# Performance work log

Hardware: AMD Instinct MI355X
Metric: run time of the kernel (lower is better)

The kernel has to match this reference:

```python
import jax, jax.numpy as jnp
import numpy as np

DIM = 1536
NH = 12
HD = DIM // NH          # 128
C = HD // 2             # 64 rotary pairs
F, H, W = 6, 20, 20
L = F * H * W           # 2400
B = 1
MAX_POS = 1024
EPS = 1e-6


def _rope_freqs():
    """[MAX_POS, C, 2, 2] rotation matrices, split [22,21,21] across f/h/w axes."""
    c0 = C - 2 * (C // 3)           # 22
    c1 = C // 3                      # 21
    pos = np.arange(MAX_POS, dtype=np.float32)
    parts = []
    for m in (c0, c1, c1):
        inv = 1.0 / (10000.0 ** (np.arange(m, dtype=np.float32) / m))
        parts.append(pos[:, None] * inv[None, :])
    ang = np.concatenate(parts, axis=1)          # [MAX_POS, C]
    cos, sin = np.cos(ang), np.sin(ang)
    # R[..., j, k]: rows [cos, -sin], [sin, cos]
    R = np.stack([np.stack([cos, -sin], -1), np.stack([sin, cos], -1)], -2)
    return jnp.asarray(R, dtype=jnp.float32)


def setup_inputs() -> dict:
    key = jax.random.key(0)
    ks = jax.random.split(key, 12)
    s = 1.0 / np.sqrt(DIM)
    lin = lambda k: (jax.random.normal(k, (DIM, DIM), jnp.float32) * s)
    return {
        "x": jax.random.normal(ks[0], (B, L, DIM), jnp.float32),
        "Wq": lin(ks[1]), "bq": jax.random.normal(ks[2], (DIM,), jnp.float32) * 0.01,
        "Wk": lin(ks[3]), "bk": jax.random.normal(ks[4], (DIM,), jnp.float32) * 0.01,
        "Wv": lin(ks[5]), "bv": jax.random.normal(ks[6], (DIM,), jnp.float32) * 0.01,
        "Wo": lin(ks[7]), "bo": jax.random.normal(ks[8], (DIM,), jnp.float32) * 0.01,
        "gq": jnp.ones((DIM,), jnp.float32),
        "gk": jnp.ones((DIM,), jnp.float32),
        "seq_lens": jnp.full((B,), L, dtype=jnp.int32),
        "grid_sizes": jnp.asarray([[F, H, W]], dtype=jnp.int32),
        "freqs": _rope_freqs(),
    }


def _rms_norm(x, g, eps=EPS):
    # WanRMSNorm: x * rsqrt(mean(x^2, -1) + eps) * weight
    return x * jax.lax.rsqrt(jnp.mean(jnp.square(x), axis=-1, keepdims=True) + eps) * g


def _rope_apply(xh, grid_sizes, freqs):
    """xh: [B, L, n, d]; freqs: [MAX_POS, c, 2, 2]. All samples share one grid."""
    b, l, n, d = xh.shape
    c = d // 2
    c0 = c - 2 * (c // 3)
    c1 = c // 3
    f, h, w = (int(v) for v in np.asarray(grid_sizes[0]))
    # build per-position 3D rotation matrices: [f*h*w, c, 2, 2]
    fa = jnp.broadcast_to(freqs[:f, :c0][:, None, None], (f, h, w, c0, 2, 2))
    fb = jnp.broadcast_to(freqs[:h, c0:c0 + c1][None, :, None], (f, h, w, c1, 2, 2))
    fc = jnp.broadcast_to(freqs[:w, c0 + c1:c][None, None, :], (f, h, w, c1, 2, 2))
    R = jnp.concatenate([fa, fb, fc], axis=3).reshape(f * h * w, c, 2, 2)
    xp = xh.reshape(b, l, n, c, 2)
    out = jnp.einsum('lcjk,blnck->blncj', R, xp)
    return out.reshape(b, l, n, d)


def reference(x, Wq, bq, Wk, bk, Wv, bv, Wo, bo, gq, gk, seq_lens, grid_sizes, freqs):
    b, l = x.shape[:2]
    q = _rms_norm(x @ Wq.T + bq, gq).reshape(b, l, NH, HD)
    k = _rms_norm(x @ Wk.T + bk, gk).reshape(b, l, NH, HD)
    v = (x @ Wv.T + bv).reshape(b, l, NH, HD)
    q = _rope_apply(q, grid_sizes, freqs)
    k = _rope_apply(k, grid_sizes, freqs)
    # full attention with key-length mask (window_size=(-1,-1))
    scores = jnp.einsum('bqnd,bknd->bnqk', q, k) / np.sqrt(HD)
    kmask = jnp.arange(l)[None, :] < seq_lens[:, None]          # [B, L]
    scores = jnp.where(kmask[:, None, None, :], scores, -1e9)
    attn = jax.nn.softmax(scores, axis=-1)
    out = jnp.einsum('bnqk,bknd->bqnd', attn, v).reshape(b, l, DIM)
    return out @ Wo.T + bo
```

## Files before the change

### kernel.cpp

```cpp
#include <hip/hip_runtime.h>
#include <hip/hip_bf16.h>
#include <stdint.h>


#define DIM  1536
#define NH   12
#define HD   128
#define LSEQ 2400
#define LPAD 2432
#define KT2  32
#define NT2  (LPAD / KT2)
#define NTH  38
#define KVH  (LPAD / 2)

typedef __attribute__((ext_vector_type(8))) short short8;
typedef __attribute__((ext_vector_type(8))) _Float16 half8;
typedef __attribute__((ext_vector_type(4))) float f32x4;
typedef unsigned short ushort_t;
typedef unsigned int   uint32;

__device__ __forceinline__ ushort_t f2bf(float f) {
  union { float f; unsigned u; } v; v.f = f;
  unsigned r = (v.u + 0x7fffu + ((v.u >> 16) & 1u)) >> 16;
  return (ushort_t)r;
}
__device__ __forceinline__ float bf2f(ushort_t h) {
  union { unsigned u; float f; } v; v.u = ((unsigned)h) << 16;
  return v.f;
}
__device__ __forceinline__ void async16(void* lds, const void* g) {
  __builtin_amdgcn_global_load_lds(
      (const __attribute__((address_space(1))) uint32*)g,
      (__attribute__((address_space(3))) uint32*)lds, 16, 0, 0);
}
__device__ __forceinline__ uint4 pack8(const float* f) {
  uint4 u;
  u.x = (uint32)f2bf(f[0]) | ((uint32)f2bf(f[1]) << 16);
  u.y = (uint32)f2bf(f[2]) | ((uint32)f2bf(f[3]) << 16);
  u.z = (uint32)f2bf(f[4]) | ((uint32)f2bf(f[5]) << 16);
  u.w = (uint32)f2bf(f[6]) | ((uint32)f2bf(f[7]) << 16);
  return u;
}

__global__ void cvt_all(const float* __restrict__ x,
                        const float* __restrict__ W0, const float* __restrict__ W1,
                        const float* __restrict__ W2, const float* __restrict__ W3,
                        ushort_t* __restrict__ xd,
                        ushort_t* __restrict__ d0, ushort_t* __restrict__ d1,
                        ushort_t* __restrict__ d2, ushort_t* __restrict__ d3)
{
  const int z = blockIdx.y;
  const int i = blockIdx.x * 256 + threadIdx.x;
  if (z == 0) {
    uint4 u = {0, 0, 0, 0};
    if (i * 8 < LSEQ * DIM) {
      float f[8];
      *(float4*)f = *(const float4*)(x + i * 8);
      *(float4*)(f + 4) = *(const float4*)(x + i * 8 + 4);
      u = pack8(f);
    }
    *(uint4*)(xd + i * 8) = u;
    return;
  }
  if (blockIdx.x >= DIM * DIM / 2048) return;
  const float* s = (z == 1) ? W0 : ((z == 2) ? W1 : ((z == 3) ? W2 : W3));
  ushort_t* d    = (z == 1) ? d0 : ((z == 2) ? d1 : ((z == 3) ? d2 : d3));
  float f[8];
  *(float4*)f = *(const float4*)(s + i * 8);
  *(float4*)(f + 4) = *(const float4*)(s + i * 8 + 4);
  *(uint4*)(d + i * 8) = pack8(f);
}

template<int OUT_F32>
__global__ __launch_bounds__(256) void gemm_bt(
    const ushort_t* __restrict__ Ap,
    const ushort_t* __restrict__ B0, const ushort_t* __restrict__ B1, const ushort_t* __restrict__ B2,
    const float* __restrict__ b0, const float* __restrict__ b1, const float* __restrict__ b2,
    void* __restrict__ D0, void* __restrict__ D1, void* __restrict__ D2,
    int Mout)
{
  const int z = blockIdx.y;
  const ushort_t* Bw  = (z == 0) ? B0 : ((z == 1) ? B1 : B2);
  const float* bias   = (z == 0) ? b0 : ((z == 1) ? b1 : b2);
  void* D             = (z == 0) ? D0 : ((z == 1) ? D1 : D2);

  const int bm = blockIdx.x / 12, bn = blockIdx.x % 12;
  const int tid = threadIdx.x;
  const int w = tid >> 6, lam = tid & 63;
  const int wr = w >> 1, wc = w & 1;
  const int lane15 = lam & 15, quad = lam >> 4;

  __shared__ __align__(16) char lds[32768];
  char* sA = lds;
  char* sB = lds + 16384;

  f32x4 acc[4][4];
#pragma unroll
  for (int i = 0; i < 4; ++i)
#pragma unroll
    for (int j = 0; j < 4; ++j) acc[i][j] = {};

  const int sm = (w * 32) + (lam >> 3);
  const int sc = (lam & 7);

  for (int k0 = 0; k0 < DIM; k0 += 64) {
    __syncthreads();
#pragma unroll
    for (int i = 0; i < 4; ++i) {
      const int li = w * 4096 + i * 1024;
      const int m = sm + i * 8;
      const int c = sc ^ (m & 7);
      async16(sA + li, Ap + (size_t)(bm * 128 + m) * DIM + k0 + c * 8);
      async16(sB + li, Bw + (size_t)(bn * 128 + m) * DIM + k0 + c * 8);
    }
    __syncthreads();
#pragma unroll
    for (int kc = 0; kc < 2; ++kc) {
      const int chunk = kc * 4 + quad;
      short8 af[4], bfr[4];
#pragma unroll
      for (int i = 0; i < 4; ++i) {
        const int m = wr * 64 + i * 16 + lane15;
        af[i] = *(const short8*)(sA + m * 128 + ((chunk ^ (m & 7)) * 16));
      }
#pragma unroll
      for (int j = 0; j < 4; ++j) {
        const int n = wc * 64 + j * 16 + lane15;
        bfr[j] = *(const short8*)(sB + n * 128 + ((chunk ^ (n & 7)) * 16));
      }
#pragma unroll
      for (int i = 0; i < 4; ++i)
#pragma unroll
        for (int j = 0; j < 4; ++j)
          acc[i][j] = __builtin_amdgcn_mfma_f32_16x16x32_bf16(af[i], bfr[j], acc[i][j], 0, 0, 0);
    }
  }

#pragma unroll
  for (int j = 0; j < 4; ++j) {
    const int n = bn * 128 + wc * 64 + j * 16 + lane15;
    const float bv = bias[n];
#pragma unroll
    for (int i = 0; i < 4; ++i) {
      const int mb = bm * 128 + wr * 64 + i * 16 + quad * 4;
#pragma unroll
      for (int r = 0; r < 4; ++r) {
        const int m = mb + r;
        const float val = acc[i][j][r] + bv;
        if (OUT_F32) {
          if (m < Mout) ((float*)D)[(size_t)m * DIM + n] = val;
        } else {
          ((ushort_t*)D)[(size_t)m * DIM + n] = f2bf(val);
        }
      }
    }
  }
}

__global__ __launch_bounds__(256) void nr_vp(
    const ushort_t* __restrict__ qpre, const ushort_t* __restrict__ kpre,
    const ushort_t* __restrict__ vbf,
    const float* __restrict__ gq, const float* __restrict__ gk,
    const float* __restrict__ freqs,
    const int* __restrict__ seq_lens, const int* __restrict__ grid_sizes,
    ushort_t* __restrict__ qh, ushort_t* __restrict__ kh,
    ushort_t* __restrict__ vp)
{
  const int bx = blockIdx.x;
  const int tid = threadIdx.x;
  __shared__ float wsum[4];
  __shared__ float srstd;
  __shared__ ushort_t tbuf[32][33];

  if (bx >= 2 * LPAD) {
    const int vb = bx - 2 * LPAD;
    const int head = vb / (NT2 * 4);
    const int rem = vb - head * (NT2 * 4);
    const int t2 = rem >> 2;
    const int d0 = (rem & 3) * 32;
    const int l0 = t2 * 32;
    const int tx = tid & 31, ty = tid >> 5;
#pragma unroll
    for (int rr = 0; rr < 4; ++rr)
      tbuf[ty * 4 + rr][tx] = vbf[(size_t)(l0 + ty * 4 + rr) * DIM + head * HD + d0 + tx];
    __syncthreads();
#pragma unroll
    for (int rr = 0; rr < 4; ++rr) {
      const int d = d0 + ty * 4 + rr;
      vp[(((size_t)head * NT2 + t2) * HD + d) * KT2 + tx] = tbuf[tx][ty * 4 + rr];
    }
    return;
  }

  const int row = bx >> 1;
  const int which = bx & 1;
  const ushort_t* src = which ? kpre : qpre;
  const float* g = which ? gk : gq;
  ushort_t* dst = which ? kh : qh;

  float s = 0.f;
  if (tid < 192) {
    uint4 u = *(const uint4*)(src + (size_t)row * DIM + tid * 8);
    const uint32 uu[4] = {u.x, u.y, u.z, u.w};
#pragma unroll
    for (int i = 0; i < 4; ++i) {
      float a = bf2f((ushort_t)(uu[i] & 0xffff));
      float b = bf2f((ushort_t)(uu[i] >> 16));
      s += a * a + b * b;
    }
  }
#pragma unroll
  for (int off = 32; off; off >>= 1) s += __shfl_down(s, off, 64);
  if ((tid & 63) == 0) wsum[tid >> 6] = s;
  __syncthreads();
  if (tid == 0)
    srstd = rsqrtf((wsum[0] + wsum[1] + wsum[2] + wsum[3]) / (float)DIM + 1e-6f);
  __syncthreads();
  const float rstd = srstd;

  const int seq = seq_lens[0];
  const int h_ = grid_sizes[1], w_ = grid_sizes[2];
  const int hw = h_ * w_;
  const int fidx = row / hw;
  const int rem = row - fidx * hw;
  const int hidx = rem / w_;
  const int widx = rem - hidx * w_;
  const bool live = row < seq;

#pragma unroll
  for (int pp = 0; pp < 3; ++pp) {
    const int p = tid + pp * 256;
    const int c = p & 63, head = p >> 6;
    const int e_in = head * HD + 2 * c;
    uint32 xin = *(const uint32*)(src + (size_t)row * DIM + e_in);
    float x0 = bf2f((ushort_t)(xin & 0xffff));
    float x1 = bf2f((ushort_t)(xin >> 16));
    float2 gg = *(const float2*)(g + e_in);
    float y0 = x0 * rstd * gg.x, y1 = x1 * rstd * gg.y;
    const int pos = (c < 22) ? fidx : ((c < 43) ? hidx : widx);
    float4 R = *(const float4*)(freqs + ((size_t)pos * 64 + c) * 4);
    float o0 = R.x * y0 + R.y * y1;
    float o1 = R.z * y0 + R.w * y1;
    uint32 op = live ? ((uint32)f2bf(o0) | ((uint32)f2bf(o1) << 16)) : 0u;
    *(uint32*)(dst + ((size_t)head * LPAD + row) * HD + 2 * c) = op;
  }
}

__global__ __launch_bounds__(256, 2) void attn6(
    const ushort_t* __restrict__ qh, const ushort_t* __restrict__ kh,
    const ushort_t* __restrict__ vp, const int* __restrict__ seq_lens,
    _Float16* __restrict__ opA, _Float16* __restrict__ opB,
    float* __restrict__ lp)
{
  const int half = blockIdx.z;
  const int head = blockIdx.y;
  const int q0 = blockIdx.x * 64;
  const int tid = threadIdx.x;
  const int w = tid >> 6, lam = tid & 63;
  const int lane15 = lam & 15, quad = lam >> 4;
  const int seq = seq_lens[0];
  _Float16* op = half ? opB : opA;

  __shared__ __align__(16) char kbuf[2][8192];
  __shared__ __align__(16) char vbuf[2][8192];
  __shared__ __align__(16) ushort_t pbuf[4][16][40];

  const ushort_t* qbase = qh + ((size_t)head * LPAD + q0 + w * 16) * HD;
  short8 qf[4];
#pragma unroll
  for (int kc = 0; kc < 4; ++kc)
    qf[kc] = *(const short8*)(qbase + lane15 * HD + kc * 32 + quad * 8);

  f32x4 o[8];
#pragma unroll
  for (int dt = 0; dt < 8; ++dt) o[dt] = {};
  float lacc[4] = {0.f, 0.f, 0.f, 0.f};

  const float scale = 0.08838834764831845f;

  const ushort_t* khh = kh + (size_t)head * LPAD * HD;
  const ushort_t* vph = vp + (size_t)head * NT2 * HD * KT2;

  const int krow0 = w * 8 + (lam >> 4);
  const int kslot = lam & 15;
  const int vrow0 = w * 32 + (lam >> 2);
  const int vslot = lam & 3;

#define STAGE(gt, b)                                                     \
  {                                                                      \
    const ushort_t* kg = khh + (size_t)(gt) * (KT2 * HD);                \
    const ushort_t* vg = vph + (size_t)(gt) * (HD * KT2);                \
    _Pragma("unroll")                                                    \
    for (int i = 0; i < 2; ++i) {                                        \
      const int li = w * 2048 + i * 1024;                                \
      const int kr = krow0 + i * 4;                                      \
      const int kc_ = kslot ^ (kr & 15);                                 \
      async16(kbuf[b] + li, kg + kr * HD + kc_ * 8);                     \
      const int vr = vrow0 + i * 16;                                     \
      const int vc = vslot ^ (vr & 3);                                   \
      async16(vbuf[b] + li, vg + vr * KT2 + vc * 8);                     \
    }                                                                    \
  }

  STAGE(half * NTH, 0)
  __syncthreads();

  for (int t = 0; t < NTH; ++t) {
    const int b = t & 1;
    const int gt = half * NTH + t;
    if (t + 1 < NTH) STAGE(gt + 1, b ^ 1)

    f32x4 S[2];
    S[0] = {}; S[1] = {};
#pragma unroll
    for (int n0 = 0; n0 < 2; ++n0)
#pragma unroll
      for (int kc = 0; kc < 4; ++kc) {
        short8 kf = *(const short8*)(kbuf[b] + (n0 * 16 + lane15) * 256 +
                                     (((kc * 4 + quad) ^ lane15) * 16));
        S[n0] = __builtin_amdgcn_mfma_f32_16x16x32_bf16(qf[kc], kf, S[n0], 0, 0, 0);
      }

#pragma unroll
    for (int n0 = 0; n0 < 2; ++n0) {
      const bool valid = (gt * KT2 + n0 * 16 + lane15) < seq;
#pragma unroll
      for (int r = 0; r < 4; ++r) {
        float e = valid ? __expf(S[n0][r] * scale - 12.0f) : 0.f;
        lacc[r] += e;
        pbuf[w][quad * 4 + r][n0 * 16 + lane15] = f2bf(e);
      }
    }
    asm volatile("s_waitcnt lgkmcnt(0)" ::: "memory");

    short8 pf = *(const short8*)(&pbuf[w][lane15][quad * 8]);
#pragma unroll
    for (int dt = 0; dt < 8; ++dt) {
      short8 vf = *(const short8*)(vbuf[b] + (dt * 16 + lane15) * 64 +
                                   ((quad ^ (lane15 & 3)) * 16));
      o[dt] = __builtin_amdgcn_mfma_f32_16x16x32_bf16(pf, vf, o[dt], 0, 0, 0);
    }
    __syncthreads();
  }
#undef STAGE

  float lrow[4], linv[4];
#pragma unroll
  for (int r = 0; r < 4; ++r) {
    float l = lacc[r];
#pragma unroll
    for (int off = 1; off < 16; off <<= 1) l += __shfl_xor(l, off, 16);
    lrow[r] = l;
    linv[r] = 1.0f / l;
  }
  if (lane15 == 0) {
#pragma unroll
    for (int r = 0; r < 4; ++r)
      lp[((size_t)half * NH + head) * LPAD + q0 + w * 16 + quad * 4 + r] = lrow[r];
  }
#pragma unroll
  for (int dt = 0; dt < 8; ++dt)
#pragma unroll
    for (int r = 0; r < 4; ++r) {
      const int m = q0 + w * 16 + quad * 4 + r;
      op[(size_t)m * DIM + head * HD + dt * 16 + lane15] =
          (_Float16)(o[dt][r] * linv[r]);
    }
}

__global__ void merge(const _Float16* __restrict__ oA, const _Float16* __restrict__ oB,
                      const float* __restrict__ lp, ushort_t* __restrict__ attno)
{
  const int i = blockIdx.x * 256 + threadIdx.x;
  const int e = i * 8;
  const int m = e / DIM;
  const int head = (e - m * DIM) >> 7;
  const float lA = lp[(size_t)head * LPAD + m];
  const float lB = lp[((size_t)NH + head) * LPAD + m];
  const float inv = 1.0f / (lA + lB);
  const float wA = lA * inv, wB = lB * inv;
  half8 a = *(const half8*)(oA + e);
  half8 b = *(const half8*)(oB + e);
  float f[8];
#pragma unroll
  for (int j = 0; j < 8; ++j) f[j] = (float)a[j] * wA + (float)b[j] * wB;
  *(uint4*)(attno + e) = pack8(f);
}

extern "C" void kernel_launch(void* const* d_in, const int* in_sizes, int n_in,
                              void* d_out, int out_size, void* d_ws, size_t ws_size,
                              hipStream_t stream)
{
  const float* x  = (const float*)d_in[0];
  const float* Wq = (const float*)d_in[1];
  const float* bq = (const float*)d_in[2];
  const float* Wk = (const float*)d_in[3];
  const float* bk = (const float*)d_in[4];
  const float* Wv = (const float*)d_in[5];
  const float* bv = (const float*)d_in[6];
  const float* Wo = (const float*)d_in[7];
  const float* bo = (const float*)d_in[8];
  const float* gq = (const float*)d_in[9];
  const float* gk = (const float*)d_in[10];
  const int* seq_lens   = (const int*)d_in[11];
  const int* grid_sizes = (const int*)d_in[12];
  const float* freqs    = (const float*)d_in[13];
  float* out = (float*)d_out;

  const size_t BUF = (size_t)LPAD * DIM * 2;
  const size_t WB  = (size_t)DIM * DIM * 2;
  char* ws = (char*)d_ws;
  dim3 blk(256);

  ushort_t* xbf  = (ushort_t*)(ws);
  ushort_t* wqb  = (ushort_t*)(ws + BUF);
  ushort_t* wkb  = (ushort_t*)(ws + BUF + WB);
  ushort_t* wvb  = (ushort_t*)(ws + BUF + 2 * WB);
  ushort_t* wob  = (ushort_t*)(ws + BUF + 3 * WB);
  ushort_t* qpre = (ushort_t*)(ws + BUF + 4 * WB);
  ushort_t* kpre = (ushort_t*)(ws + 2 * BUF + 4 * WB);
  ushort_t* qh   = (ushort_t*)(ws + 3 * BUF + 4 * WB);
  ushort_t* kh   = (ushort_t*)(ws + 4 * BUF + 4 * WB);
  ushort_t* vbf  = (ushort_t*)(ws + 5 * BUF + 4 * WB);
  ushort_t* vp    = xbf;
  ushort_t* attno = xbf;
  _Float16* opA = (_Float16*)qpre;
  _Float16* opB = (_Float16*)vbf;
  float*    lp  = (float*)wvb;

  cvt_all<<<dim3(LPAD * DIM / 2048, 5), blk, 0, stream>>>(
      x, Wq, Wk, Wv, Wo, xbf, wqb, wkb, wvb, wob);
  gemm_bt<0><<<dim3(228, 3), blk, 0, stream>>>(
      xbf, wqb, wkb, wvb, bq, bk, bv, qpre, kpre, vbf, 0);
  nr_vp<<<dim3(2 * LPAD + NH * NT2 * 4), blk, 0, stream>>>(
      qpre, kpre, vbf, gq, gk, freqs, seq_lens, grid_sizes, qh, kh, vp);
  attn6<<<dim3(LPAD / 64, NH, 2), blk, 0, stream>>>(
      qh, kh, vp, seq_lens, opA, opB, lp);
  merge<<<dim3(LPAD * DIM / 2048), blk, 0, stream>>>(opA, opB, lp, attno);
  gemm_bt<1><<<dim3(228, 1), blk, 0, stream>>>(
      attno, wob, wob, wob, bo, bo, bo, out, out, out, LSEQ);
}
```

Before: 296.9 us.

## Double query tile per wave and split keys into four chunks

```diff
diff --git a/kernel.cpp b/kernel.cpp
--- a/kernel.cpp
+++ b/kernel.cpp
@@ -10,8 +10,7 @@
 #define LPAD 2432
 #define KT2  32
 #define NT2  (LPAD / KT2)
-#define NTH  38
-#define KVH  (LPAD / 2)
+#define NTQ  19
 
 typedef __attribute__((ext_vector_type(8))) short short8;
 typedef __attribute__((ext_vector_type(8))) _Float16 half8;
@@ -246,35 +245,40 @@
   }
 }
 
-__global__ __launch_bounds__(256, 2) void attn6(
+__global__ __launch_bounds__(256, 3) void attn7(
     const ushort_t* __restrict__ qh, const ushort_t* __restrict__ kh,
     const ushort_t* __restrict__ vp, const int* __restrict__ seq_lens,
-    _Float16* __restrict__ opA, _Float16* __restrict__ opB,
+    _Float16* __restrict__ op0, _Float16* __restrict__ op1,
+    _Float16* __restrict__ op2, _Float16* __restrict__ op3,
     float* __restrict__ lp)
 {
-  const int half = blockIdx.z;
+  const int qz = blockIdx.z;
   const int head = blockIdx.y;
-  const int q0 = blockIdx.x * 64;
+  const int q0 = blockIdx.x * 128;
   const int tid = threadIdx.x;
   const int w = tid >> 6, lam = tid & 63;
   const int lane15 = lam & 15, quad = lam >> 4;
   const int seq = seq_lens[0];
-  _Float16* op = half ? opB : opA;
+  _Float16* op = (qz == 0) ? op0 : ((qz == 1) ? op1 : ((qz == 2) ? op2 : op3));
 
   __shared__ __align__(16) char kbuf[2][8192];
   __shared__ __align__(16) char vbuf[2][8192];
-  __shared__ __align__(16) ushort_t pbuf[4][16][40];
-
-  const ushort_t* qbase = qh + ((size_t)head * LPAD + q0 + w * 16) * HD;
-  short8 qf[4];
-#pragma unroll
-  for (int kc = 0; kc < 4; ++kc)
-    qf[kc] = *(const short8*)(qbase + lane15 * HD + kc * 32 + quad * 8);
-
-  f32x4 o[8];
-#pragma unroll
-  for (int dt = 0; dt < 8; ++dt) o[dt] = {};
-  float lacc[4] = {0.f, 0.f, 0.f, 0.f};
+  __shared__ __align__(16) ushort_t pbuf[4][32][40];
+
+  const ushort_t* qbase = qh + ((size_t)head * LPAD + q0 + w * 32) * HD;
+  short8 qf[2][4];
+#pragma unroll
+  for (int qt = 0; qt < 2; ++qt)
+#pragma unroll
+    for (int kc = 0; kc < 4; ++kc)
+      qf[qt][kc] = *(const short8*)(qbase + (qt * 16 + lane15) * HD + kc * 32 + quad * 8);
+
+  f32x4 o[2][8];
+#pragma unroll
+  for (int qt = 0; qt < 2; ++qt)
+#pragma unroll
+    for (int dt = 0; dt < 8; ++dt) o[qt][dt] = {};
+  float lacc[2][4] = {};
 
   const float scale = 0.08838834764831845f;
 
@@ -283,8 +287,6 @@
 
   const int krow0 = w * 8 + (lam >> 4);
   const int kslot = lam & 15;
-  const int vrow0 = w * 32 + (lam >> 2);
-  const int vslot = lam & 3;
 
 #define STAGE(gt, b)                                                     \
   {                                                                      \
@@ -296,94 +298,114 @@
       const int kr = krow0 + i * 4;                                      \
       const int kc_ = kslot ^ (kr & 15);                                 \
       async16(kbuf[b] + li, kg + kr * HD + kc_ * 8);                     \
-      const int vr = vrow0 + i * 16;                                     \
-      const int vc = vslot ^ (vr & 3);                                   \
-      async16(vbuf[b] + li, vg + vr * KT2 + vc * 8);                     \
+      const int G = w * 128 + i * 64 + lam;                              \
+      const int l_ = (G >> 2) & 15;                                      \
+      const int cc = (G & 3) ^ (l_ & 3);                                 \
+      const int d_ = ((G >> 6) << 4) + l_;                               \
+      async16(vbuf[b] + li, vg + d_ * KT2 + cc * 8);                     \
     }                                                                    \
   }
 
-  STAGE(half * NTH, 0)
+  const int tbase = qz * NTQ;
+  STAGE(tbase, 0)
   __syncthreads();
 
-  for (int t = 0; t < NTH; ++t) {
+  for (int t = 0; t < NTQ; ++t) {
     const int b = t & 1;
-    const int gt = half * NTH + t;
-    if (t + 1 < NTH) STAGE(gt + 1, b ^ 1)
-
-    f32x4 S[2];
-    S[0] = {}; S[1] = {};
+    const int gt = tbase + t;
+    if (t + 1 < NTQ) STAGE(gt + 1, b ^ 1)
+
+    f32x4 S[2][2];
+    S[0][0] = {}; S[0][1] = {}; S[1][0] = {}; S[1][1] = {};
 #pragma unroll
     for (int n0 = 0; n0 < 2; ++n0)
 #pragma unroll
       for (int kc = 0; kc < 4; ++kc) {
         short8 kf = *(const short8*)(kbuf[b] + (n0 * 16 + lane15) * 256 +
                                      (((kc * 4 + quad) ^ lane15) * 16));
-        S[n0] = __builtin_amdgcn_mfma_f32_16x16x32_bf16(qf[kc], kf, S[n0], 0, 0, 0);
+#pragma unroll
+        for (int qt = 0; qt < 2; ++qt)
+          S[qt][n0] = __builtin_amdgcn_mfma_f32_16x16x32_bf16(qf[qt][kc], kf, S[qt][n0], 0, 0, 0);
       }
 
 #pragma unroll
     for (int n0 = 0; n0 < 2; ++n0) {
       const bool valid = (gt * KT2 + n0 * 16 + lane15) < seq;
 #pragma unroll
+      for (int qt = 0; qt < 2; ++qt)
+#pragma unroll
+        for (int r = 0; r < 4; ++r) {
+          float e = valid ? __expf(S[qt][n0][r] * scale - 12.0f) : 0.f;
+          lacc[qt][r] += e;
+          pbuf[w][qt * 16 + quad * 4 + r][n0 * 16 + lane15] = f2bf(e);
+        }
+    }
+    asm volatile("s_waitcnt lgkmcnt(0)" ::: "memory");
+
+    short8 pf[2];
+#pragma unroll
+    for (int qt = 0; qt < 2; ++qt)
+      pf[qt] = *(const short8*)(&pbuf[w][qt * 16 + lane15][quad * 8]);
+#pragma unroll
+    for (int dt = 0; dt < 8; ++dt) {
+      short8 vf = *(const short8*)(vbuf[b] + dt * 1024 +
+                                   (lane15 * 4 + (quad ^ (lane15 & 3))) * 16);
+#pragma unroll
+      for (int qt = 0; qt < 2; ++qt)
+        o[qt][dt] = __builtin_amdgcn_mfma_f32_16x16x32_bf16(pf[qt], vf, o[qt][dt], 0, 0, 0);
+    }
+    __syncthreads();
+  }
+#undef STAGE
+
+#pragma unroll
+  for (int qt = 0; qt < 2; ++qt) {
+    float lrow[4], linv[4];
+#pragma unroll
+    for (int r = 0; r < 4; ++r) {
+      float l = lacc[qt][r];
+#pragma unroll
+      for (int off = 1; off < 16; off <<= 1) l += __shfl_xor(l, off, 16);
+      lrow[r] = l;
+      linv[r] = 1.0f / l;
+    }
+    if (lane15 == 0) {
+#pragma unroll
+      for (int r = 0; r < 4; ++r)
+        lp[((size_t)qz * NH + head) * LPAD + q0 + w * 32 + qt * 16 + quad * 4 + r] = lrow[r];
+    }
+#pragma unroll
+    for (int dt = 0; dt < 8; ++dt)
+#pragma unroll
       for (int r = 0; r < 4; ++r) {
-        float e = valid ? __expf(S[n0][r] * scale - 12.0f) : 0.f;
-        lacc[r] += e;
-        pbuf[w][quad * 4 + r][n0 * 16 + lane15] = f2bf(e);
+        const int m = q0 + w * 32 + qt * 16 + quad * 4 + r;
+        op[(size_t)m * DIM + head * HD + dt * 16 + lane15] =
+            (_Float16)(o[qt][dt][r] * linv[r]);
       }
-    }
-    asm volatile("s_waitcnt lgkmcnt(0)" ::: "memory");
-
-    short8 pf = *(const short8*)(&pbuf[w][lane15][quad * 8]);
-#pragma unroll
-    for (int dt = 0; dt < 8; ++dt) {
-      short8 vf = *(const short8*)(vbuf[b] + (dt * 16 + lane15) * 64 +
-                                   ((quad ^ (lane15 & 3)) * 16));
-      o[dt] = __builtin_amdgcn_mfma_f32_16x16x32_bf16(pf, vf, o[dt], 0, 0, 0);
-    }
-    __syncthreads();
-  }
-#undef STAGE
-
-  float lrow[4], linv[4];
-#pragma unroll
-  for (int r = 0; r < 4; ++r) {
-    float l = lacc[r];
-#pragma unroll
-    for (int off = 1; off < 16; off <<= 1) l += __shfl_xor(l, off, 16);
-    lrow[r] = l;
-    linv[r] = 1.0f / l;
-  }
-  if (lane15 == 0) {
-#pragma unroll
-    for (int r = 0; r < 4; ++r)
-      lp[((size_t)half * NH + head) * LPAD + q0 + w * 16 + quad * 4 + r] = lrow[r];
-  }
-#pragma unroll
-  for (int dt = 0; dt < 8; ++dt)
-#pragma unroll
-    for (int r = 0; r < 4; ++r) {
-      const int m = q0 + w * 16 + quad * 4 + r;
-      op[(size_t)m * DIM + head * HD + dt * 16 + lane15] =
-          (_Float16)(o[dt][r] * linv[r]);
-    }
-}
-
-__global__ void merge(const _Float16* __restrict__ oA, const _Float16* __restrict__ oB,
+  }
+}
+
+__global__ void merge(const _Float16* __restrict__ o0, const _Float16* __restrict__ o1,
+                      const _Float16* __restrict__ o2, const _Float16* __restrict__ o3,
                       const float* __restrict__ lp, ushort_t* __restrict__ attno)
 {
   const int i = blockIdx.x * 256 + threadIdx.x;
   const int e = i * 8;
   const int m = e / DIM;
   const int head = (e - m * DIM) >> 7;
-  const float lA = lp[(size_t)head * LPAD + m];
-  const float lB = lp[((size_t)NH + head) * LPAD + m];
-  const float inv = 1.0f / (lA + lB);
-  const float wA = lA * inv, wB = lB * inv;
-  half8 a = *(const half8*)(oA + e);
-  half8 b = *(const half8*)(oB + e);
+  float l[4];
+#pragma unroll
+  for (int h = 0; h < 4; ++h) l[h] = lp[((size_t)h * NH + head) * LPAD + m];
+  const float inv = 1.0f / (l[0] + l[1] + l[2] + l[3]);
+  half8 a = *(const half8*)(o0 + e);
+  half8 b = *(const half8*)(o1 + e);
+  half8 c = *(const half8*)(o2 + e);
+  half8 d = *(const half8*)(o3 + e);
+  const float w0 = l[0] * inv, w1 = l[1] * inv, w2 = l[2] * inv, w3 = l[3] * inv;
   float f[8];
 #pragma unroll
-  for (int j = 0; j < 8; ++j) f[j] = (float)a[j] * wA + (float)b[j] * wB;
+  for (int j = 0; j < 8; ++j)
+    f[j] = (float)a[j] * w0 + (float)b[j] * w1 + (float)c[j] * w2 + (float)d[j] * w3;
   *(uint4*)(attno + e) = pack8(f);
 }
 
@@ -424,8 +446,10 @@
   ushort_t* vbf  = (ushort_t*)(ws + 5 * BUF + 4 * WB);
   ushort_t* vp    = xbf;
   ushort_t* attno = xbf;
-  _Float16* opA = (_Float16*)qpre;
-  _Float16* opB = (_Float16*)vbf;
+  _Float16* op0 = (_Float16*)qpre;
+  _Float16* op1 = (_Float16*)kpre;
+  _Float16* op2 = (_Float16*)vbf;
+  _Float16* op3 = (_Float16*)wqb;
   float*    lp  = (float*)wvb;
 
   cvt_all<<<dim3(LPAD * DIM / 2048, 5), blk, 0, stream>>>(
@@ -434,9 +458,9 @@
       xbf, wqb, wkb, wvb, bq, bk, bv, qpre, kpre, vbf, 0);
   nr_vp<<<dim3(2 * LPAD + NH * NT2 * 4), blk, 0, stream>>>(
       qpre, kpre, vbf, gq, gk, freqs, seq_lens, grid_sizes, qh, kh, vp);
-  attn6<<<dim3(LPAD / 64, NH, 2), blk, 0, stream>>>(
-      qh, kh, vp, seq_lens, opA, opB, lp);
-  merge<<<dim3(LPAD * DIM / 2048), blk, 0, stream>>>(opA, opB, lp, attno);
+  attn7<<<dim3(LPAD / 128, NH, 4), blk, 0, stream>>>(
+      qh, kh, vp, seq_lens, op0, op1, op2, op3, lp);
+  merge<<<dim3(LPAD * DIM / 2048), blk, 0, stream>>>(op0, op1, op2, op3, lp, attno);
   gemm_bt<1><<<dim3(228, 1), blk, 0, stream>>>(
       attno, wob, wob, wob, bo, bo, bo, out, out, out, LSEQ);
 }
```

Result: no change. 296.4 us (-0.2%).
